# Optimization experiments

Hardware: AMD Instinct MI355X
Metric: run time of the kernel (lower is better)

## Reference

```python
import jax, jax.numpy as jnp
import numpy as np

NUM_HEADS = 8
IN_DIM = 384
HEAD_DIM = IN_DIM // NUM_HEADS  # 48


def setup_inputs() -> dict:
    key = jax.random.key(0)
    ks = jax.random.split(key, 6)
    B, N, M, C = 4, 4096, 1024, 384
    q_x = jax.random.normal(ks[0], (B, N, C), dtype=jnp.float32)
    kv_x = jax.random.normal(ks[1], (B, M, C), dtype=jnp.float32)
    s = C ** -0.5  # fan-in style init scale
    Wq = jax.random.normal(ks[2], (C, IN_DIM), dtype=jnp.float32) * s
    Wkv = jax.random.normal(ks[3], (C, 2 * IN_DIM), dtype=jnp.float32) * s
    Wproj = jax.random.normal(ks[4], (IN_DIM, IN_DIM), dtype=jnp.float32) * (IN_DIM ** -0.5)
    bproj = jnp.zeros((IN_DIM,), dtype=jnp.float32)
    return {"q_x": q_x, "kv_x": kv_x, "Wq": Wq, "Wkv": Wkv, "Wproj": Wproj, "bproj": bproj}


def reference(q_x, kv_x, Wq, Wkv, Wproj, bproj):
    B, N, C = q_x.shape
    M = kv_x.shape[1]
    scale = HEAD_DIM ** -0.5
    # q: [B, H, N, hd]
    q = (q_x @ Wq).reshape(B, N, NUM_HEADS, HEAD_DIM).transpose(0, 2, 1, 3)
    # k, v: [B, H, M, hd]
    kv = (kv_x @ Wkv).reshape(B, M, 2, NUM_HEADS, HEAD_DIM).transpose(2, 0, 3, 1, 4)
    k, v = kv[0], kv[1]
    # attention scores [B, H, N, M]
    attn = jax.nn.softmax(jnp.einsum('bhnd,bhmd->bhnm', q, k) * scale, axis=-1)
    x = jnp.einsum('bhnm,bhmd->bhnd', attn, v)  # [B, H, N, hd]
    x = x.transpose(0, 2, 1, 3).reshape(B, N, IN_DIM)
    x = x @ Wproj + bproj
    # sr_ratio == 1 residual: add raw q projection back
    q_res = q.transpose(0, 2, 1, 3).reshape(B, N, IN_DIM)
    return q_res + x
```

## Files before the change

kernel.cpp:

```cpp
#include <hip/hip_runtime.h>
#include <hip/hip_bf16.h>
#include <math.h>

#define B_ 4
#define N_ 4096
#define M_ 1024
#define C_ 384
#define NH_ 8
#define HD_ 48

typedef float f32x4 __attribute__((ext_vector_type(4)));
typedef short bf16x8 __attribute__((ext_vector_type(8)));

__device__ __forceinline__ unsigned short f2bf(float x) {
    unsigned int u = __builtin_bit_cast(unsigned int, x);
    return (unsigned short)((u + 0x7FFFu + ((u >> 16) & 1u)) >> 16);
}
__device__ __forceinline__ unsigned short f2bf_trunc(float x) {
    return (unsigned short)(__builtin_bit_cast(unsigned int, x) >> 16);
}
__device__ __forceinline__ float fast_exp2(float x) {
#if __has_builtin(__builtin_amdgcn_exp2f)
    return __builtin_amdgcn_exp2f(x);
#else
    return exp2f(x);
#endif
}

#define QSCALE 0.20823490983597203f

__global__ __launch_bounds__(256)
void conv_act(const float* __restrict__ a, unsigned short* __restrict__ da,
              const float* __restrict__ b, unsigned short* __restrict__ db)
{
    size_t i4 = (size_t)blockIdx.x * 256 + threadIdx.x;
    const float* src; unsigned short* dst;
    if (i4 < 1572864u) { src = a; dst = da; }
    else { src = b; dst = db; i4 -= 1572864u; }
    float4 v = *(const float4*)&src[i4 * 4];
    uint2 pk;
    pk.x = (unsigned int)f2bf(v.x) | ((unsigned int)f2bf(v.y) << 16);
    pk.y = (unsigned int)f2bf(v.z) | ((unsigned int)f2bf(v.w) << 16);
    *(uint2*)&dst[i4 * 4] = pk;
}

__global__ __launch_bounds__(256)
void transpose_w3(const float* __restrict__ Wq, const float* __restrict__ Wkv,
                  const float* __restrict__ Wproj,
                  unsigned short* __restrict__ Wq_t, unsigned short* __restrict__ Wkv_t,
                  unsigned short* __restrict__ Wproj_t)
{
    __shared__ unsigned short T[64 * 72];
    const int tid = threadIdx.x;
    int bid = blockIdx.x;
    const float* W; unsigned short* Wt; int N, kt, nt;
    if (bid < 36)       { W = Wq;    Wt = Wq_t;    N = 384; kt = bid / 6;  nt = bid - kt * 6; }
    else if (bid < 108) { bid -= 36;  W = Wkv;   Wt = Wkv_t;   N = 768; kt = bid / 12; nt = bid - kt * 12; }
    else                { bid -= 108; W = Wproj; Wt = Wproj_t; N = 384; kt = bid / 6;  nt = bid - kt * 6; }
    const int k0 = kt * 64, n0 = nt * 64;

    #pragma unroll
    for (int it = 0; it < 4; ++it) {
        int k = it * 16 + (tid >> 4);
        int n4 = (tid & 15) * 4;
        float4 v = *(const float4*)&W[(size_t)(k0 + k) * N + n0 + n4];
        T[(n4 + 0) * 72 + k] = f2bf(v.x);
        T[(n4 + 1) * 72 + k] = f2bf(v.y);
        T[(n4 + 2) * 72 + k] = f2bf(v.z);
        T[(n4 + 3) * 72 + k] = f2bf(v.w);
    }
    __syncthreads();
    #pragma unroll
    for (int i = 0; i < 2; ++i) {
        int s = tid + 256 * i;
        int n = s >> 3, part = s & 7;
        *(uint4*)&Wt[(size_t)(n0 + n) * C_ + k0 + part * 8] = *(const uint4*)&T[n * 72 + part * 8];
    }
}

__global__ __launch_bounds__(256)
void gemm_bf16(const unsigned short* __restrict__ A, const unsigned short* __restrict__ Wt,
               float* __restrict__ out0,
               unsigned short* __restrict__ bf0, unsigned short* __restrict__ bf1,
               const float* __restrict__ addend, const float* __restrict__ bias,
               int mode)
{
    __shared__ unsigned short As[128 * 72];
    __shared__ unsigned short Ws[64 * 72];
    const int tid = threadIdx.x;
    const int wave = tid >> 6;
    const int lane = tid & 63;
    const int ln = lane & 15;
    const int quad = lane >> 4;
    const int row0 = blockIdx.x * 128;
    const int col0 = blockIdx.y * 64;

    f32x4 acc[2][4];
    #pragma unroll
    for (int rt = 0; rt < 2; ++rt)
        #pragma unroll
        for (int t = 0; t < 4; ++t) acc[rt][t] = (f32x4){0.f, 0.f, 0.f, 0.f};

    for (int kk = 0; kk < C_; kk += 64) {
        __syncthreads();
        #pragma unroll
        for (int i = 0; i < 4; ++i) {
            int s = tid + 256 * i;
            int r = s >> 3, part = s & 7;
            *(uint4*)&As[r * 72 + part * 8] =
                *(const uint4*)&A[(size_t)(row0 + r) * C_ + kk + part * 8];
        }
        #pragma unroll
        for (int i = 0; i < 2; ++i) {
            int s = tid + 256 * i;
            int n = s >> 3, part = s & 7;
            *(uint4*)&Ws[n * 72 + part * 8] =
                *(const uint4*)&Wt[(size_t)(col0 + n) * C_ + kk + part * 8];
        }
        __syncthreads();

        bf16x8 af[2][2];
        #pragma unroll
        for (int rt = 0; rt < 2; ++rt) {
            const unsigned short* Ap = &As[(wave * 32 + rt * 16 + ln) * 72];
            af[rt][0] = *(const bf16x8*)&Ap[quad * 8];
            af[rt][1] = *(const bf16x8*)&Ap[32 + quad * 8];
        }
        #pragma unroll
        for (int t = 0; t < 4; ++t) {
            const unsigned short* Wp = &Ws[(t * 16 + ln) * 72];
            bf16x8 b0 = *(const bf16x8*)&Wp[quad * 8];
            bf16x8 b1 = *(const bf16x8*)&Wp[32 + quad * 8];
            #pragma unroll
            for (int rt = 0; rt < 2; ++rt) {
                acc[rt][t] = __builtin_amdgcn_mfma_f32_16x16x32_bf16(af[rt][0], b0, acc[rt][t], 0, 0, 0);
                acc[rt][t] = __builtin_amdgcn_mfma_f32_16x16x32_bf16(af[rt][1], b1, acc[rt][t], 0, 0, 0);
            }
        }
    }

    #pragma unroll
    for (int rt = 0; rt < 2; ++rt) {
        #pragma unroll
        for (int t = 0; t < 4; ++t) {
            int gcol = col0 + t * 16 + ln;
            #pragma unroll
            for (int r = 0; r < 4; ++r) {
                int grow = row0 + wave * 32 + rt * 16 + quad * 4 + r;
                float v = acc[rt][t][r];
                if (mode == 0) {
                    out0[(size_t)grow * C_ + gcol] = v;
                    int b = grow >> 12, n = grow & (N_ - 1);
                    int h = gcol / HD_, d = gcol - h * HD_;
                    bf0[(((size_t)(b * NH_ + h) * N_) + n) * HD_ + d] = f2bf(v * QSCALE);
                } else if (mode == 1) {
                    int b = grow >> 10, m = grow & (M_ - 1);
                    if (gcol < C_) {
                        int h = gcol / HD_, d = gcol - h * HD_;
                        bf0[(((size_t)(b * NH_ + h) * M_) + m) * HD_ + d] = f2bf(v);
                    } else {
                        int c2 = gcol - C_;
                        int h = c2 / HD_, d = c2 - h * HD_;
                        bf1[(((size_t)(b * NH_ + h) * HD_) + d) * M_ + m] = f2bf(v);
                    }
                } else {
                    size_t idx = (size_t)grow * C_ + gcol;
                    out0[idx] = v + addend[idx] + bias[gcol];
                }
            }
        }
    }
}

__global__ __launch_bounds__(256)
void attn_mfma(const unsigned short* __restrict__ qbf,
               const unsigned short* __restrict__ kbf,
               const unsigned short* __restrict__ vbf,
               unsigned short* __restrict__ of)
{
    __shared__ unsigned short QP[64 * 72];
    __shared__ unsigned short Ks[64 * 72];
    __shared__ unsigned short Vt[64 * 72];

    const int tid = threadIdx.x;
    const int wave = tid >> 6;
    const int lane = tid & 63;
    const int ln = lane & 15;
    const int quad = lane >> 4;
    const int bh = blockIdx.y;
    const int n0 = blockIdx.x * 64;

    uint4 z4; z4.x = z4.y = z4.z = z4.w = 0u;
    for (int e = tid; e < 576; e += 256) {
        *(uint4*)&QP[e * 8] = z4;
        *(uint4*)&Ks[e * 8] = z4;
        *(uint4*)&Vt[e * 8] = z4;
    }
    __syncthreads();
    if (tid < 64) Vt[48 * 72 + tid] = 0x3F80;
    const unsigned short* qsrc = qbf + ((size_t)bh * N_ + n0) * HD_;
    for (int e = tid; e < 384; e += 256) {
        int r = e / 6, part = e - r * 6;
        *(uint4*)&QP[r * 72 + part * 8] = *(const uint4*)&qsrc[r * HD_ + part * 8];
    }
    __syncthreads();

    const unsigned short* Qw = &QP[(wave * 16 + ln) * 72];
    bf16x8 aq0 = *(const bf16x8*)&Qw[quad * 8];
    bf16x8 aq1 = *(const bf16x8*)&Qw[32 + quad * 8];

    f32x4 O[4];
    #pragma unroll
    for (int t = 0; t < 4; ++t) O[t] = (f32x4){0.f, 0.f, 0.f, 0.f};

    const unsigned short* ksrc = kbf + (size_t)bh * M_ * HD_;
    const unsigned short* vsrc = vbf + (size_t)bh * HD_ * M_;
    unsigned short* Pw = &QP[wave * 16 * 72];
    const int phys_r = (ln & 3) * 4 + (ln >> 2);
    const unsigned short* Pr = &QP[(wave * 16 + phys_r) * 72];

    for (int mt = 0; mt < M_ / 64; ++mt) {
        __syncthreads();
        const unsigned short* kp = ksrc + (size_t)mt * 64 * HD_;
        for (int e = tid; e < 384; e += 256) {
            int r = e / 6, part = e - r * 6;
            *(uint4*)&Ks[r * 72 + part * 8] = *(const uint4*)&kp[r * HD_ + part * 8];
        }
        for (int e = tid; e < 384; e += 256) {
            int d = e >> 3, part = e & 7;
            *(uint4*)&Vt[d * 72 + part * 8] =
                *(const uint4*)&vsrc[(size_t)d * M_ + mt * 64 + part * 8];
        }
        __syncthreads();

        f32x4 S[4];
        #pragma unroll
        for (int t = 0; t < 4; ++t) S[t] = (f32x4){0.f, 0.f, 0.f, 0.f};
        #pragma unroll
        for (int t = 0; t < 4; ++t) {
            const unsigned short* Kp = &Ks[(t * 16 + ln) * 72];
            bf16x8 b0 = *(const bf16x8*)&Kp[quad * 8];
            S[t] = __builtin_amdgcn_mfma_f32_16x16x32_bf16(aq0, b0, S[t], 0, 0, 0);
            bf16x8 b1 = *(const bf16x8*)&Kp[32 + quad * 8];
            S[t] = __builtin_amdgcn_mfma_f32_16x16x32_bf16(aq1, b1, S[t], 0, 0, 0);
        }

        #pragma unroll
        for (int t = 0; t < 4; ++t)
            #pragma unroll
            for (int r = 0; r < 4; ++r)
                Pw[(r * 4 + quad) * 72 + t * 16 + ln] = f2bf_trunc(fast_exp2(S[t][r]));

        bf16x8 pa0 = *(const bf16x8*)&Pr[quad * 8];
        bf16x8 pa1 = *(const bf16x8*)&Pr[32 + quad * 8];
        #pragma unroll
        for (int ot = 0; ot < 4; ++ot) {
            const unsigned short* Vp = &Vt[(ot * 16 + ln) * 72];
            bf16x8 b0 = *(const bf16x8*)&Vp[quad * 8];
            O[ot] = __builtin_amdgcn_mfma_f32_16x16x32_bf16(pa0, b0, O[ot], 0, 0, 0);
            bf16x8 b1 = *(const bf16x8*)&Vp[32 + quad * 8];
            O[ot] = __builtin_amdgcn_mfma_f32_16x16x32_bf16(pa1, b1, O[ot], 0, 0, 0);
        }
    }

    const int b = bh >> 3, h = bh & 7;
    float inv[4];
    #pragma unroll
    for (int r = 0; r < 4; ++r)
        inv[r] = 1.0f / __shfl(O[3][r], lane & 48);
    #pragma unroll
    for (int ot = 0; ot < 3; ++ot) {
        int gcol = h * HD_ + ot * 16 + ln;
        #pragma unroll
        for (int r = 0; r < 4; ++r) {
            int grow = n0 + wave * 16 + quad * 4 + r;
            of[((size_t)b * N_ + grow) * C_ + gcol] = f2bf(O[ot][r] * inv[r]);
        }
    }
}

extern "C" void kernel_launch(void* const* d_in, const int* in_sizes, int n_in,
                              void* d_out, int out_size, void* d_ws, size_t ws_size,
                              hipStream_t stream) {
    const float* q_x   = (const float*)d_in[0];
    const float* kv_x  = (const float*)d_in[1];
    const float* Wq    = (const float*)d_in[2];
    const float* Wkv   = (const float*)d_in[3];
    const float* Wproj = (const float*)d_in[4];
    const float* bproj = (const float*)d_in[5];
    float* out = (float*)d_out;

    float* qf = (float*)d_ws;
    unsigned short* base = (unsigned short*)(qf + 6291456);
    unsigned short* qx_bf   = base;
    unsigned short* kvx_bf  = qx_bf  + 6291456;
    unsigned short* qbf     = kvx_bf + 1572864;
    unsigned short* kbf     = qbf    + 6291456;
    unsigned short* vbf     = kbf    + 1572864;
    unsigned short* Wq_t    = vbf    + 1572864;
    unsigned short* Wkv_t   = Wq_t   + 147456;
    unsigned short* Wproj_t = Wkv_t  + 294912;
    unsigned short* of      = qx_bf;

    dim3 blk(256);

    conv_act<<<dim3(7680), blk, 0, stream>>>(q_x, qx_bf, kv_x, kvx_bf);
    transpose_w3<<<dim3(144), blk, 0, stream>>>(Wq, Wkv, Wproj, Wq_t, Wkv_t, Wproj_t);

    gemm_bf16<<<dim3(128, 6), blk, 0, stream>>>(
        qx_bf, Wq_t, qf, qbf, nullptr, nullptr, nullptr, 0);

    gemm_bf16<<<dim3(32, 12), blk, 0, stream>>>(
        kvx_bf, Wkv_t, nullptr, kbf, vbf, nullptr, nullptr, 1);

    attn_mfma<<<dim3(64, 32), blk, 0, stream>>>(qbf, kbf, vbf, of);

    gemm_bf16<<<dim3(128, 6), blk, 0, stream>>>(
        of, Wproj_t, out, nullptr, nullptr, qf, bproj, 2);
}
```

Before: 208.4 us.

## Rework GEMMs with resident weight tile and register-direct attention loads

The GEMM now keeps the whole 64-column weight slab in LDS and streams A rows straight from global memory into MFMA operands, with no per-k-tile barriers. Epilogues write vectorized packed bf16 or float4. The q residual is stored as bf16 instead of fp32, which halves that traffic at a small cost in precision. Attention drops the shared K/V staging: each wave loads K and V fragments directly from global, handles 32 query rows, computes row sums in registers instead of through a ones column in V, and uses the block grid ordered by head first to improve K/V cache reuse.

Measured after the change: 204.0 us. 1.02x faster.

```diff
diff --git a/kernel.cpp b/kernel.cpp
--- a/kernel.cpp
+++ b/kernel.cpp
@@ -19,12 +19,21 @@
 __device__ __forceinline__ unsigned short f2bf_trunc(float x) {
     return (unsigned short)(__builtin_bit_cast(unsigned int, x) >> 16);
 }
+__device__ __forceinline__ float bf2f(unsigned short x) {
+    return __builtin_bit_cast(float, (unsigned int)x << 16);
+}
 __device__ __forceinline__ float fast_exp2(float x) {
 #if __has_builtin(__builtin_amdgcn_exp2f)
     return __builtin_amdgcn_exp2f(x);
 #else
     return exp2f(x);
 #endif
+}
+__device__ __forceinline__ uint2 pack4_rne(float a, float b, float c, float d) {
+    uint2 r;
+    r.x = (unsigned int)f2bf(a) | ((unsigned int)f2bf(b) << 16);
+    r.y = (unsigned int)f2bf(c) | ((unsigned int)f2bf(d) << 16);
+    return r;
 }
 
 #define QSCALE 0.20823490983597203f
@@ -38,10 +47,7 @@
     if (i4 < 1572864u) { src = a; dst = da; }
     else { src = b; dst = db; i4 -= 1572864u; }
     float4 v = *(const float4*)&src[i4 * 4];
-    uint2 pk;
-    pk.x = (unsigned int)f2bf(v.x) | ((unsigned int)f2bf(v.y) << 16);
-    pk.y = (unsigned int)f2bf(v.z) | ((unsigned int)f2bf(v.w) << 16);
-    *(uint2*)&dst[i4 * 4] = pk;
+    *(uint2*)&dst[i4 * 4] = pack4_rne(v.x, v.y, v.z, v.w);
 }
 
 __global__ __launch_bounds__(256)
@@ -79,14 +85,13 @@
 }
 
 __global__ __launch_bounds__(256)
-void gemm_bf16(const unsigned short* __restrict__ A, const unsigned short* __restrict__ Wt,
-               float* __restrict__ out0,
-               unsigned short* __restrict__ bf0, unsigned short* __restrict__ bf1,
-               const float* __restrict__ addend, const float* __restrict__ bias,
-               int mode)
+void gemm_hyb(const unsigned short* __restrict__ A, const unsigned short* __restrict__ Wt,
+              float* __restrict__ out0,
+              unsigned short* __restrict__ bf0, unsigned short* __restrict__ bf1,
+              const unsigned short* __restrict__ addend, const float* __restrict__ bias,
+              int mode)
 {
-    __shared__ unsigned short As[128 * 72];
-    __shared__ unsigned short Ws[64 * 72];
+    __shared__ unsigned short Ws[64 * 392];
     const int tid = threadIdx.x;
     const int wave = tid >> 6;
     const int lane = tid & 63;
@@ -95,188 +100,192 @@
     const int row0 = blockIdx.x * 128;
     const int col0 = blockIdx.y * 64;
 
+    for (int i = tid; i < 3072; i += 256) {
+        int n = i / 48, part = i - n * 48;
+        *(uint4*)&Ws[n * 392 + part * 8] = *(const uint4*)&Wt[(size_t)(col0 + n) * C_ + part * 8];
+    }
+    __syncthreads();
+
     f32x4 acc[2][4];
     #pragma unroll
     for (int rt = 0; rt < 2; ++rt)
         #pragma unroll
-        for (int t = 0; t < 4; ++t) acc[rt][t] = (f32x4){0.f, 0.f, 0.f, 0.f};
-
-    for (int kk = 0; kk < C_; kk += 64) {
-        __syncthreads();
-        #pragma unroll
-        for (int i = 0; i < 4; ++i) {
-            int s = tid + 256 * i;
-            int r = s >> 3, part = s & 7;
-            *(uint4*)&As[r * 72 + part * 8] =
-                *(const uint4*)&A[(size_t)(row0 + r) * C_ + kk + part * 8];
-        }
-        #pragma unroll
-        for (int i = 0; i < 2; ++i) {
-            int s = tid + 256 * i;
-            int n = s >> 3, part = s & 7;
-            *(uint4*)&Ws[n * 72 + part * 8] =
-                *(const uint4*)&Wt[(size_t)(col0 + n) * C_ + kk + part * 8];
-        }
-        __syncthreads();
-
-        bf16x8 af[2][2];
-        #pragma unroll
-        for (int rt = 0; rt < 2; ++rt) {
-            const unsigned short* Ap = &As[(wave * 32 + rt * 16 + ln) * 72];
-            af[rt][0] = *(const bf16x8*)&Ap[quad * 8];
-            af[rt][1] = *(const bf16x8*)&Ap[32 + quad * 8];
-        }
-        #pragma unroll
-        for (int t = 0; t < 4; ++t) {
-            const unsigned short* Wp = &Ws[(t * 16 + ln) * 72];
-            bf16x8 b0 = *(const bf16x8*)&Wp[quad * 8];
-            bf16x8 b1 = *(const bf16x8*)&Wp[32 + quad * 8];
-            #pragma unroll
-            for (int rt = 0; rt < 2; ++rt) {
-                acc[rt][t] = __builtin_amdgcn_mfma_f32_16x16x32_bf16(af[rt][0], b0, acc[rt][t], 0, 0, 0);
-                acc[rt][t] = __builtin_amdgcn_mfma_f32_16x16x32_bf16(af[rt][1], b1, acc[rt][t], 0, 0, 0);
+        for (int ct = 0; ct < 4; ++ct) acc[rt][ct] = (f32x4){0.f, 0.f, 0.f, 0.f};
+
+    const unsigned short* arow0 = A + (size_t)(row0 + wave * 32 + ln) * C_;
+    const unsigned short* arow1 = arow0 + 16 * C_;
+
+    #pragma unroll
+    for (int kc = 0; kc < 12; ++kc) {
+        bf16x8 b0 = *(const bf16x8*)(arow0 + kc * 32 + quad * 8);
+        bf16x8 b1 = *(const bf16x8*)(arow1 + kc * 32 + quad * 8);
+        #pragma unroll
+        for (int ct = 0; ct < 4; ++ct) {
+            bf16x8 aw = *(const bf16x8*)&Ws[(ct * 16 + ln) * 392 + kc * 32 + quad * 8];
+            acc[0][ct] = __builtin_amdgcn_mfma_f32_16x16x32_bf16(aw, b0, acc[0][ct], 0, 0, 0);
+            acc[1][ct] = __builtin_amdgcn_mfma_f32_16x16x32_bf16(aw, b1, acc[1][ct], 0, 0, 0);
+        }
+    }
+
+    #pragma unroll
+    for (int rt = 0; rt < 2; ++rt) {
+        int grow = row0 + wave * 32 + rt * 16 + ln;
+        #pragma unroll
+        for (int ct = 0; ct < 4; ++ct) {
+            int gcb = col0 + ct * 16 + quad * 4;
+            f32x4 v = acc[rt][ct];
+            if (mode == 0) {
+                *(uint2*)&bf1[(size_t)grow * C_ + gcb] = pack4_rne(v[0], v[1], v[2], v[3]);
+                int b = grow >> 12, n = grow & (N_ - 1);
+                int h = gcb / HD_, d = gcb - h * HD_;
+                *(uint2*)&bf0[(((size_t)(b * NH_ + h) * N_) + n) * HD_ + d] =
+                    pack4_rne(v[0] * QSCALE, v[1] * QSCALE, v[2] * QSCALE, v[3] * QSCALE);
+            } else if (mode == 1) {
+                int b = grow >> 10, m = grow & (M_ - 1);
+                if (col0 < C_) {
+                    int h = gcb / HD_, d = gcb - h * HD_;
+                    *(uint2*)&bf0[(((size_t)(b * NH_ + h) * M_) + m) * HD_ + d] =
+                        pack4_rne(v[0], v[1], v[2], v[3]);
+                } else {
+                    int c2 = gcb - C_;
+                    int h = c2 / HD_, d = c2 - h * HD_;
+                    size_t base = ((size_t)(b * NH_ + h) * HD_ + d) * M_ + m;
+                    #pragma unroll
+                    for (int r = 0; r < 4; ++r) bf1[base + (size_t)r * M_] = f2bf(v[r]);
+                }
+            } else {
+                size_t idx = (size_t)grow * C_ + gcb;
+                uint2 ad = *(const uint2*)&addend[idx];
+                float4 bi = *(const float4*)&bias[gcb];
+                float4 o;
+                o.x = v[0] + bf2f((unsigned short)(ad.x & 0xFFFF)) + bi.x;
+                o.y = v[1] + bf2f((unsigned short)(ad.x >> 16))    + bi.y;
+                o.z = v[2] + bf2f((unsigned short)(ad.y & 0xFFFF)) + bi.z;
+                o.w = v[3] + bf2f((unsigned short)(ad.y >> 16))    + bi.w;
+                *(float4*)&out0[idx] = o;
             }
         }
     }
-
-    #pragma unroll
-    for (int rt = 0; rt < 2; ++rt) {
-        #pragma unroll
-        for (int t = 0; t < 4; ++t) {
-            int gcol = col0 + t * 16 + ln;
-            #pragma unroll
-            for (int r = 0; r < 4; ++r) {
-                int grow = row0 + wave * 32 + rt * 16 + quad * 4 + r;
-                float v = acc[rt][t][r];
-                if (mode == 0) {
-                    out0[(size_t)grow * C_ + gcol] = v;
-                    int b = grow >> 12, n = grow & (N_ - 1);
-                    int h = gcol / HD_, d = gcol - h * HD_;
-                    bf0[(((size_t)(b * NH_ + h) * N_) + n) * HD_ + d] = f2bf(v * QSCALE);
-                } else if (mode == 1) {
-                    int b = grow >> 10, m = grow & (M_ - 1);
-                    if (gcol < C_) {
-                        int h = gcol / HD_, d = gcol - h * HD_;
-                        bf0[(((size_t)(b * NH_ + h) * M_) + m) * HD_ + d] = f2bf(v);
-                    } else {
-                        int c2 = gcol - C_;
-                        int h = c2 / HD_, d = c2 - h * HD_;
-                        bf1[(((size_t)(b * NH_ + h) * HD_) + d) * M_ + m] = f2bf(v);
-                    }
-                } else {
-                    size_t idx = (size_t)grow * C_ + gcol;
-                    out0[idx] = v + addend[idx] + bias[gcol];
-                }
-            }
-        }
-    }
-}
-
-__global__ __launch_bounds__(256)
+}
+
+__global__ __launch_bounds__(256, 4)
 void attn_mfma(const unsigned short* __restrict__ qbf,
                const unsigned short* __restrict__ kbf,
                const unsigned short* __restrict__ vbf,
                unsigned short* __restrict__ of)
 {
-    __shared__ unsigned short QP[64 * 72];
-    __shared__ unsigned short Ks[64 * 72];
-    __shared__ unsigned short Vt[64 * 72];
+    __shared__ unsigned short P[4][32 * 72];
 
     const int tid = threadIdx.x;
     const int wave = tid >> 6;
     const int lane = tid & 63;
     const int ln = lane & 15;
     const int quad = lane >> 4;
-    const int bh = blockIdx.y;
-    const int n0 = blockIdx.x * 64;
-
-    uint4 z4; z4.x = z4.y = z4.z = z4.w = 0u;
-    for (int e = tid; e < 576; e += 256) {
-        *(uint4*)&QP[e * 8] = z4;
-        *(uint4*)&Ks[e * 8] = z4;
-        *(uint4*)&Vt[e * 8] = z4;
-    }
-    __syncthreads();
-    if (tid < 64) Vt[48 * 72 + tid] = 0x3F80;
-    const unsigned short* qsrc = qbf + ((size_t)bh * N_ + n0) * HD_;
-    for (int e = tid; e < 384; e += 256) {
-        int r = e / 6, part = e - r * 6;
-        *(uint4*)&QP[r * 72 + part * 8] = *(const uint4*)&qsrc[r * HD_ + part * 8];
-    }
-    __syncthreads();
-
-    const unsigned short* Qw = &QP[(wave * 16 + ln) * 72];
-    bf16x8 aq0 = *(const bf16x8*)&Qw[quad * 8];
-    bf16x8 aq1 = *(const bf16x8*)&Qw[32 + quad * 8];
-
-    f32x4 O[4];
-    #pragma unroll
-    for (int t = 0; t < 4; ++t) O[t] = (f32x4){0.f, 0.f, 0.f, 0.f};
-
-    const unsigned short* ksrc = kbf + (size_t)bh * M_ * HD_;
-    const unsigned short* vsrc = vbf + (size_t)bh * HD_ * M_;
-    unsigned short* Pw = &QP[wave * 16 * 72];
-    const int phys_r = (ln & 3) * 4 + (ln >> 2);
-    const unsigned short* Pr = &QP[(wave * 16 + phys_r) * 72];
+    const int bh = blockIdx.x;
+    const int n0w = blockIdx.y * 128 + wave * 32;
+
+    const bf16x8 zero8 = (bf16x8){0, 0, 0, 0, 0, 0, 0, 0};
+
+    bf16x8 qb[2][2];
+    #pragma unroll
+    for (int qt = 0; qt < 2; ++qt) {
+        const unsigned short* qp = qbf + ((size_t)bh * N_ + n0w + qt * 16 + ln) * HD_;
+        qb[qt][0] = *(const bf16x8*)(qp + quad * 8);
+        qb[qt][1] = *(const bf16x8*)(qp + 32 + quad * 8);
+        if (quad >= 2) qb[qt][1] = zero8;
+    }
+
+    f32x4 O[3][2];
+    #pragma unroll
+    for (int ot = 0; ot < 3; ++ot)
+        #pragma unroll
+        for (int qt = 0; qt < 2; ++qt) O[ot][qt] = (f32x4){0.f, 0.f, 0.f, 0.f};
+    float rs[2] = {0.f, 0.f};
+
+    const unsigned short* kb = kbf + (size_t)bh * M_ * HD_;
+    const unsigned short* vb = vbf + (size_t)bh * HD_ * M_;
+    unsigned short* Pw = &P[wave][0];
 
     for (int mt = 0; mt < M_ / 64; ++mt) {
         __syncthreads();
-        const unsigned short* kp = ksrc + (size_t)mt * 64 * HD_;
-        for (int e = tid; e < 384; e += 256) {
-            int r = e / 6, part = e - r * 6;
-            *(uint4*)&Ks[r * 72 + part * 8] = *(const uint4*)&kp[r * HD_ + part * 8];
-        }
-        for (int e = tid; e < 384; e += 256) {
-            int d = e >> 3, part = e & 7;
-            *(uint4*)&Vt[d * 72 + part * 8] =
-                *(const uint4*)&vsrc[(size_t)d * M_ + mt * 64 + part * 8];
-        }
-        __syncthreads();
-
-        f32x4 S[4];
-        #pragma unroll
-        for (int t = 0; t < 4; ++t) S[t] = (f32x4){0.f, 0.f, 0.f, 0.f};
-        #pragma unroll
-        for (int t = 0; t < 4; ++t) {
-            const unsigned short* Kp = &Ks[(t * 16 + ln) * 72];
-            bf16x8 b0 = *(const bf16x8*)&Kp[quad * 8];
-            S[t] = __builtin_amdgcn_mfma_f32_16x16x32_bf16(aq0, b0, S[t], 0, 0, 0);
-            bf16x8 b1 = *(const bf16x8*)&Kp[32 + quad * 8];
-            S[t] = __builtin_amdgcn_mfma_f32_16x16x32_bf16(aq1, b1, S[t], 0, 0, 0);
-        }
-
+
+        f32x4 S[4][2];
         #pragma unroll
         for (int t = 0; t < 4; ++t)
             #pragma unroll
-            for (int r = 0; r < 4; ++r)
-                Pw[(r * 4 + quad) * 72 + t * 16 + ln] = f2bf_trunc(fast_exp2(S[t][r]));
-
-        bf16x8 pa0 = *(const bf16x8*)&Pr[quad * 8];
-        bf16x8 pa1 = *(const bf16x8*)&Pr[32 + quad * 8];
-        #pragma unroll
-        for (int ot = 0; ot < 4; ++ot) {
-            const unsigned short* Vp = &Vt[(ot * 16 + ln) * 72];
-            bf16x8 b0 = *(const bf16x8*)&Vp[quad * 8];
-            O[ot] = __builtin_amdgcn_mfma_f32_16x16x32_bf16(pa0, b0, O[ot], 0, 0, 0);
-            bf16x8 b1 = *(const bf16x8*)&Vp[32 + quad * 8];
-            O[ot] = __builtin_amdgcn_mfma_f32_16x16x32_bf16(pa1, b1, O[ot], 0, 0, 0);
-        }
+            for (int qt = 0; qt < 2; ++qt) S[t][qt] = (f32x4){0.f, 0.f, 0.f, 0.f};
+        #pragma unroll
+        for (int t = 0; t < 4; ++t) {
+            const unsigned short* kp = kb + (size_t)(mt * 64 + t * 16 + ln) * HD_;
+            bf16x8 k0 = *(const bf16x8*)(kp + quad * 8);
+            bf16x8 k1 = *(const bf16x8*)(kp + 32 + quad * 8);
+            if (quad >= 2) k1 = zero8;
+            #pragma unroll
+            for (int qt = 0; qt < 2; ++qt) {
+                S[t][qt] = __builtin_amdgcn_mfma_f32_16x16x32_bf16(k0, qb[qt][0], S[t][qt], 0, 0, 0);
+                S[t][qt] = __builtin_amdgcn_mfma_f32_16x16x32_bf16(k1, qb[qt][1], S[t][qt], 0, 0, 0);
+            }
+        }
+
+        #pragma unroll
+        for (int qt = 0; qt < 2; ++qt)
+            #pragma unroll
+            for (int t = 0; t < 4; ++t) {
+                float p0 = fast_exp2(S[t][qt][0]);
+                float p1 = fast_exp2(S[t][qt][1]);
+                float p2 = fast_exp2(S[t][qt][2]);
+                float p3 = fast_exp2(S[t][qt][3]);
+                rs[qt] += (p0 + p1) + (p2 + p3);
+                uint2 pk;
+                pk.x = (unsigned int)f2bf_trunc(p0) | ((unsigned int)f2bf_trunc(p1) << 16);
+                pk.y = (unsigned int)f2bf_trunc(p2) | ((unsigned int)f2bf_trunc(p3) << 16);
+                *(uint2*)&Pw[(qt * 16 + ln) * 72 + t * 16 + quad * 4] = pk;
+            }
+
+        bf16x8 va[3][2];
+        #pragma unroll
+        for (int ot = 0; ot < 3; ++ot) {
+            const unsigned short* vp = vb + (size_t)(ot * 16 + ln) * M_ + mt * 64;
+            va[ot][0] = *(const bf16x8*)(vp + quad * 8);
+            va[ot][1] = *(const bf16x8*)(vp + 32 + quad * 8);
+        }
+
+        bf16x8 pb[2][2];
+        #pragma unroll
+        for (int qt = 0; qt < 2; ++qt) {
+            const unsigned short* Pr = &Pw[(qt * 16 + ln) * 72];
+            pb[qt][0] = *(const bf16x8*)(Pr + quad * 8);
+            pb[qt][1] = *(const bf16x8*)(Pr + 32 + quad * 8);
+        }
+        #pragma unroll
+        for (int ot = 0; ot < 3; ++ot)
+            #pragma unroll
+            for (int qt = 0; qt < 2; ++qt) {
+                O[ot][qt] = __builtin_amdgcn_mfma_f32_16x16x32_bf16(va[ot][0], pb[qt][0], O[ot][qt], 0, 0, 0);
+                O[ot][qt] = __builtin_amdgcn_mfma_f32_16x16x32_bf16(va[ot][1], pb[qt][1], O[ot][qt], 0, 0, 0);
+            }
+    }
+
+    float inv[2];
+    #pragma unroll
+    for (int qt = 0; qt < 2; ++qt) {
+        float x = rs[qt];
+        x += __shfl_xor(x, 16);
+        x += __shfl_xor(x, 32);
+        inv[qt] = 1.0f / x;
     }
 
     const int b = bh >> 3, h = bh & 7;
-    float inv[4];
-    #pragma unroll
-    for (int r = 0; r < 4; ++r)
-        inv[r] = 1.0f / __shfl(O[3][r], lane & 48);
-    #pragma unroll
-    for (int ot = 0; ot < 3; ++ot) {
-        int gcol = h * HD_ + ot * 16 + ln;
-        #pragma unroll
-        for (int r = 0; r < 4; ++r) {
-            int grow = n0 + wave * 16 + quad * 4 + r;
-            of[((size_t)b * N_ + grow) * C_ + gcol] = f2bf(O[ot][r] * inv[r]);
-        }
-    }
+    #pragma unroll
+    for (int ot = 0; ot < 3; ++ot)
+        #pragma unroll
+        for (int qt = 0; qt < 2; ++qt) {
+            size_t grow = (size_t)b * N_ + n0w + qt * 16 + ln;
+            int gcol = h * HD_ + ot * 16 + quad * 4;
+            *(uint2*)&of[grow * C_ + gcol] =
+                pack4_rne(O[ot][qt][0] * inv[qt], O[ot][qt][1] * inv[qt],
+                          O[ot][qt][2] * inv[qt], O[ot][qt][3] * inv[qt]);
+        }
 }
 
 extern "C" void kernel_launch(void* const* d_in, const int* in_sizes, int n_in,
@@ -290,14 +299,13 @@
     const float* bproj = (const float*)d_in[5];
     float* out = (float*)d_out;
 
-    float* qf = (float*)d_ws;
-    unsigned short* base = (unsigned short*)(qf + 6291456);
-    unsigned short* qx_bf   = base;
+    unsigned short* qx_bf   = (unsigned short*)d_ws;
     unsigned short* kvx_bf  = qx_bf  + 6291456;
     unsigned short* qbf     = kvx_bf + 1572864;
     unsigned short* kbf     = qbf    + 6291456;
     unsigned short* vbf     = kbf    + 1572864;
-    unsigned short* Wq_t    = vbf    + 1572864;
+    unsigned short* qres    = vbf    + 1572864;
+    unsigned short* Wq_t    = qres   + 6291456;
     unsigned short* Wkv_t   = Wq_t   + 147456;
     unsigned short* Wproj_t = Wkv_t  + 294912;
     unsigned short* of      = qx_bf;
@@ -307,14 +315,14 @@
     conv_act<<<dim3(7680), blk, 0, stream>>>(q_x, qx_bf, kv_x, kvx_bf);
     transpose_w3<<<dim3(144), blk, 0, stream>>>(Wq, Wkv, Wproj, Wq_t, Wkv_t, Wproj_t);
 
-    gemm_bf16<<<dim3(128, 6), blk, 0, stream>>>(
-        qx_bf, Wq_t, qf, qbf, nullptr, nullptr, nullptr, 0);
-
-    gemm_bf16<<<dim3(32, 12), blk, 0, stream>>>(
+    gemm_hyb<<<dim3(128, 6), blk, 0, stream>>>(
+        qx_bf, Wq_t, nullptr, qbf, qres, nullptr, nullptr, 0);
+
+    gemm_hyb<<<dim3(32, 12), blk, 0, stream>>>(
         kvx_bf, Wkv_t, nullptr, kbf, vbf, nullptr, nullptr, 1);
 
-    attn_mfma<<<dim3(64, 32), blk, 0, stream>>>(qbf, kbf, vbf, of);
-
-    gemm_bf16<<<dim3(128, 6), blk, 0, stream>>>(
-        of, Wproj_t, out, nullptr, nullptr, qf, bproj, 2);
-}
+    attn_mfma<<<dim3(32, 32), blk, 0, stream>>>(qbf, kbf, vbf, of);
+
+    gemm_hyb<<<dim3(128, 6), blk, 0, stream>>>(
+        of, Wproj_t, out, nullptr, nullptr, qres, bproj, 2);
+}
```
